# Kernel tuning notes

Hardware: AMD Instinct MI355X
Metric: run time of the kernel (lower is better)

The kernel has to match this reference:

```python
import jax, jax.numpy as jnp
import numpy as np

EMBED_DIM = 1024
NUM_HEADS = 16
HEAD_DIM = EMBED_DIM // NUM_HEADS


def setup_inputs() -> dict:
    key = jax.random.key(0)
    ks = jax.random.split(key, 7)
    B, S, E = 2, 2048, EMBED_DIM
    # xavier_uniform bound for square [E, E] weight
    bound = float(np.sqrt(6.0 / (E + E)))
    mkw = lambda k: jax.random.uniform(k, (E, E), jnp.float32, -bound, bound)
    return {
        "query": jax.random.normal(ks[0], (B, S, E), jnp.float32),
        "key": jax.random.normal(ks[1], (B, S, E), jnp.float32),
        "value": jax.random.normal(ks[2], (B, S, E), jnp.float32),
        "Wq": mkw(ks[3]),
        "Wk": mkw(ks[4]),
        "Wv": mkw(ks[5]),
        "Wo": mkw(ks[6]),
    }


def reference(query, key, value, Wq, Wk, Wv, Wo):
    # Chunked sigmoid attention: since sigmoid has no cross-key normalization
    # and all projections are bias-free linear maps, summing per-KV-chunk
    # partial outputs is mathematically identical to the full computation:
    #   out = (sigmoid(scale * Q K^T) @ V) @ Wo^T
    B, L, E = query.shape
    H, D = NUM_HEADS, HEAD_DIM
    scale = D ** -0.5
    q = (query @ Wq.T).reshape(B, L, H, D) * scale   # [B,L,H,D]
    k = (key @ Wk.T).reshape(B, -1, H, D)            # [B,S,H,D]
    v = (value @ Wv.T).reshape(B, -1, H, D)          # [B,S,H,D]
    scores = jax.nn.sigmoid(jnp.einsum('blhd,bshd->bhls', q, k))  # [B,H,L,S]
    o = jnp.einsum('bhls,bshd->blhd', scores, v).reshape(B, L, E)
    return o @ Wo.T
```

## Files before the change

kernel.cpp:

```cpp
#include <hip/hip_runtime.h>

typedef float f32x4 __attribute__((ext_vector_type(4)));
typedef float f32x16 __attribute__((ext_vector_type(16)));
typedef __bf16 bf16x4 __attribute__((ext_vector_type(4)));
typedef __bf16 bf16x8 __attribute__((ext_vector_type(8)));

constexpr int E = 1024;
constexpr int S = 2048;
constexpr int Bsz = 2;
constexpr int H = 16;
constexpr int Dh = 64;
constexpr int M = Bsz * S;
constexpr int E2 = 2048;

#define GLOAD_LDS16(g, l)                                                                 \
  __builtin_amdgcn_global_load_lds((const __attribute__((address_space(1))) void*)(g),    \
                                   (__attribute__((address_space(3))) void*)(l), 16, 0, 0)

__device__ __forceinline__ unsigned pk2(float a, float b) {
  union { __bf16 h[2]; unsigned u; } r;
  r.h[0] = (__bf16)a; r.h[1] = (__bf16)b;
  return r.u;
}

__global__ __launch_bounds__(256) void convert_bf16(
    const float* __restrict__ q, const float* __restrict__ k,
    const float* __restrict__ v, const float* __restrict__ wq,
    const float* __restrict__ wk, const float* __restrict__ wv,
    const float* __restrict__ wo, __bf16* __restrict__ aq,
    __bf16* __restrict__ ak, __bf16* __restrict__ av,
    __bf16* __restrict__ wqkv, __bf16* __restrict__ wob) {
  const int id = blockIdx.y;
  const float* src;
  __bf16* dst;
  int n;
  float scale = 1.0f;
  switch (id) {
    case 0: src = q;  dst = aq;             n = M * E; break;
    case 1: src = k;  dst = ak;             n = M * E; break;
    case 2: src = v;  dst = av;             n = M * E; break;
    case 3: src = wq; dst = wqkv;           n = E * E; scale = -0.18033688f; break;
    case 4: src = wk; dst = wqkv + E * E;   n = E * E; break;
    case 5: src = wv; dst = wqkv + 2 * E * E; n = E * E; break;
    default: src = wo; dst = wob;           n = E * E; break;
  }
  const int stride = gridDim.x * 256 * 8;
  for (int i = (blockIdx.x * 256 + threadIdx.x) * 8; i < n; i += stride) {
    f32x4 a = *reinterpret_cast<const f32x4*>(&src[i]);
    f32x4 b = *reinterpret_cast<const f32x4*>(&src[i + 4]);
    bf16x8 o;
    o[0] = (__bf16)(a[0] * scale); o[1] = (__bf16)(a[1] * scale);
    o[2] = (__bf16)(a[2] * scale); o[3] = (__bf16)(a[3] * scale);
    o[4] = (__bf16)(b[0] * scale); o[5] = (__bf16)(b[1] * scale);
    o[6] = (__bf16)(b[2] * scale); o[7] = (__bf16)(b[3] * scale);
    *reinterpret_cast<bf16x8*>(&dst[i]) = o;
  }
}

template <int TM, int MODE, int KS>
__global__ __launch_bounds__(256) void gemm_bf16nt(
    const __bf16* __restrict__ A0, const __bf16* __restrict__ A1,
    const __bf16* __restrict__ A2, const __bf16* __restrict__ Bw,
    void* __restrict__ C0, void* __restrict__ C1, void* __restrict__ C2) {
  constexpr int MI = TM / 32;
  __shared__ __bf16 As[TM][64];
  __shared__ __bf16 Bs[128][64];

  const int t    = threadIdx.x;
  const int lane = t & 63;
  const int wid  = t >> 6;
  const int wr   = (wid >> 1) * (TM / 2);
  const int wc   = (wid & 1) * 64;
  const int r16  = lane & 15;
  const int tm   = blockIdx.y * TM;
  const int tn   = blockIdx.x * 128;
  const int which = tn >> 10;

  const __bf16* Ab = (MODE == 0) ? (which == 0 ? A0 : which == 1 ? A1 : A2) : A0;

  f32x4 acc[MI][4] = {};

  for (int kt = 0; kt < KS / 64; ++kt) {
    const int k0  = kt * 64;
    const int k0b = k0 & 1023;
    __syncthreads();
    constexpr int ACH = TM / 8;
    constexpr int NCH = ACH + 16;
#pragma unroll
    for (int c = wid; c < NCH; c += 4) {
      const bool isA = c < ACH;
      const int cc   = isA ? c : c - ACH;
      const int L    = cc * 1024 + lane * 16;
      const int row  = L >> 7;
      const int sw   = ((L >> 4) & 7) ^ (row & 7);
      const __bf16* src = isA ? &Ab[(size_t)(tm + row) * KS + k0 + sw * 8]
                              : &Bw[(size_t)(tn + row) * 1024 + k0b + sw * 8];
      char* dst = (isA ? (char*)As : (char*)Bs) + cc * 1024;
      GLOAD_LDS16(src, dst);
    }
    __syncthreads();
#pragma unroll
    for (int kc = 0; kc < 2; ++kc) {
      bf16x8 af[MI], bfv[4];
#pragma unroll
      for (int mi = 0; mi < MI; ++mi) {
        int row = wr + mi * 16 + r16;
        int g   = (kc * 4 + (lane >> 4)) ^ (row & 7);
        af[mi] = *reinterpret_cast<const bf16x8*>(&As[row][g * 8]);
      }
#pragma unroll
      for (int ni = 0; ni < 4; ++ni) {
        int row = wc + ni * 16 + r16;
        int g   = (kc * 4 + (lane >> 4)) ^ (row & 7);
        bfv[ni] = *reinterpret_cast<const bf16x8*>(&Bs[row][g * 8]);
      }
#pragma unroll
      for (int mi = 0; mi < MI; ++mi)
#pragma unroll
        for (int ni = 0; ni < 4; ++ni)
          acc[mi][ni] = __builtin_amdgcn_mfma_f32_16x16x32_bf16(af[mi], bfv[ni],
                                                                acc[mi][ni], 0, 0, 0);
    }
  }

#pragma unroll
  for (int mi = 0; mi < MI; ++mi) {
#pragma unroll
    for (int ni = 0; ni < 4; ++ni) {
#pragma unroll
      for (int j = 0; j < 4; ++j) {
        float v = acc[mi][ni][j];
        int m = tm + wr + mi * 16 + ((lane >> 4) << 2) + j;
        int n = tn + wc + ni * 16 + r16;
        if constexpr (MODE == 0) {
          int nl = n & 1023;
          int b = m >> 11, s = m & 2047, h = nl >> 6, d = nl & 63;
          __bf16* Cout = which == 0 ? (__bf16*)C0 : which == 1 ? (__bf16*)C1
                                                              : (__bf16*)C2;
          if (which < 2) {
            Cout[((size_t)(b * H + h) * S + s) * Dh + d] = (__bf16)v;
          } else {
            int ssw = (s & ~12) | ((s & 4) << 1) | ((s & 8) >> 1);
            Cout[((size_t)(b * H + h) * Dh + d) * S + ssw] = (__bf16)v;
          }
        } else {
          ((float*)C0)[(size_t)m * E + n] = v;
        }
      }
    }
  }
}

__global__ __launch_bounds__(128, 4) void attn_sigmoid(const __bf16* __restrict__ Q,
                                                       const __bf16* __restrict__ K,
                                                       const __bf16* __restrict__ Vt,
                                                       __bf16* __restrict__ O) {
  __shared__ char smem[16384];

  const int t    = threadIdx.x;
  const int lane = t & 63;
  const int qgrp = t >> 6;
  const int l31  = lane & 31;
  const int hh   = lane >> 5;
  const int qt   = blockIdx.x >> 1;
  const int ss   = blockIdx.x & 1;
  const int q0   = qt * 64;
  const int h    = blockIdx.y;
  const int b    = blockIdx.z;

  const __bf16* Qh = Q + (size_t)(b * H + h) * S * Dh;
  const __bf16* Kh = K + (size_t)(b * H + h) * S * Dh;
  const __bf16* Vh = Vt + (size_t)(b * H + h) * Dh * S;

  const __bf16* kSrc = Kh + (size_t)(ss * 1024 + (lane >> 3)) * Dh +
                       (((lane & 7) ^ (lane >> 3)) * 8);
  const __bf16* vSrc = Vh + (size_t)(lane >> 2) * S + ss * 1024 +
                       (((lane & 3) ^ ((lane >> 3) & 3)) * 8);

  auto stage = [&](int it, int buf) {
    char* dst = smem + buf * 8192;
    if (qgrp == 0) {
#pragma unroll
      for (int j = 0; j < 4; ++j)
        GLOAD_LDS16(kSrc + it * 2048 + j * 512, dst + j * 1024);
    } else {
#pragma unroll
      for (int j = 0; j < 4; ++j)
        GLOAD_LDS16(vSrc + it * 32 + (size_t)j * 16 * S, dst + 4096 + j * 1024);
    }
  };

  bf16x8 Qf[4];
#pragma unroll
  for (int kc = 0; kc < 4; ++kc)
    Qf[kc] = *reinterpret_cast<const bf16x8*>(
        &Qh[(size_t)(q0 + qgrp * 32 + l31) * Dh + kc * 16 + hh * 8]);

  stage(0, 0);
  stage(1, 1);

  f32x16 ot0 = {}, ot1 = {};

#pragma unroll 2
  for (int it = 0; it < 32; ++it) {
    const int buf = it & 1;
    if (it + 1 < 32) {
      asm volatile("s_waitcnt vmcnt(4)" ::: "memory");
    } else {
      asm volatile("s_waitcnt vmcnt(0)" ::: "memory");
    }
    __builtin_amdgcn_s_barrier();
    __builtin_amdgcn_sched_barrier(0);

    const __bf16* Kb = (const __bf16*)(smem + buf * 8192);
    const __bf16* Vb = (const __bf16*)(smem + buf * 8192 + 4096);

    bf16x8 kf[4], vf[4];
#pragma unroll
    for (int kc = 0; kc < 4; ++kc) {
      int x = (2 * kc + hh) ^ (l31 & 7);
      kf[kc] = *reinterpret_cast<const bf16x8*>(&Kb[l31 * 64 + x * 8]);
    }
#pragma unroll
    for (int kc2 = 0; kc2 < 2; ++kc2)
#pragma unroll
      for (int dblk = 0; dblk < 2; ++dblk) {
        int row = dblk * 32 + l31;
        int x   = (2 * kc2 + hh) ^ ((l31 >> 1) & 3);
        vf[kc2 * 2 + dblk] = *reinterpret_cast<const bf16x8*>(&Vb[row * 32 + x * 8]);
      }

    f32x16 sacc = {};
    __builtin_amdgcn_s_setprio(1);
#pragma unroll
    for (int kc = 0; kc < 4; ++kc)
      sacc = __builtin_amdgcn_mfma_f32_32x32x16_bf16(kf[kc], Qf[kc], sacc, 0, 0, 0);
    __builtin_amdgcn_s_setprio(0);

    bf16x8 F[2];
    {
      union { unsigned u[4]; bf16x8 v; } fu[2];
#pragma unroll
      for (int kc2 = 0; kc2 < 2; ++kc2) {
#pragma unroll
        for (int jj = 0; jj < 4; ++jj) {
          float ya = sacc[kc2 * 8 + 2 * jj];
          float yb = sacc[kc2 * 8 + 2 * jj + 1];
          float pa = __builtin_amdgcn_rcpf(1.0f + __builtin_amdgcn_exp2f(ya));
          float pb = __builtin_amdgcn_rcpf(1.0f + __builtin_amdgcn_exp2f(yb));
          fu[kc2].u[jj] = pk2(pa, pb);
        }
        F[kc2] = fu[kc2].v;
      }
    }

    __builtin_amdgcn_s_setprio(1);
    ot0 = __builtin_amdgcn_mfma_f32_32x32x16_bf16(vf[0], F[0], ot0, 0, 0, 0);
    ot1 = __builtin_amdgcn_mfma_f32_32x32x16_bf16(vf[1], F[0], ot1, 0, 0, 0);
    ot0 = __builtin_amdgcn_mfma_f32_32x32x16_bf16(vf[2], F[1], ot0, 0, 0, 0);
    ot1 = __builtin_amdgcn_mfma_f32_32x32x16_bf16(vf[3], F[1], ot1, 0, 0, 0);
    __builtin_amdgcn_s_setprio(0);

    __builtin_amdgcn_sched_barrier(0);
    __builtin_amdgcn_s_barrier();
    if (it + 2 < 32) stage(it + 2, buf);
  }

  __bf16* Os = (__bf16*)smem;
  {
    int row = qgrp * 32 + l31;
#pragma unroll
    for (int dblk = 0; dblk < 2; ++dblk)
#pragma unroll
      for (int rp = 0; rp < 4; ++rp) {
        int r  = rp * 4;
        int g  = dblk * 4 + rp;
        int by = row * 128 + ((g ^ (row & 7)) * 16) + hh * 8;
        float a0 = dblk ? ot1[r]     : ot0[r];
        float a1 = dblk ? ot1[r + 1] : ot0[r + 1];
        float a2 = dblk ? ot1[r + 2] : ot0[r + 2];
        float a3 = dblk ? ot1[r + 3] : ot0[r + 3];
        unsigned long long val =
            (unsigned long long)pk2(a0, a1) | ((unsigned long long)pk2(a2, a3) << 32);
        *reinterpret_cast<unsigned long long*>((char*)Os + by) = val;
      }
  }
  __syncthreads();
#pragma unroll
  for (int i = 0; i < 4; ++i) {
    int c   = i * 128 + t;
    int row = c >> 3;
    int ch  = c & 7;
    bf16x8 v = *reinterpret_cast<const bf16x8*>(
        (char*)Os + row * 128 + ((ch ^ (row & 7)) * 16));
    *reinterpret_cast<bf16x8*>(
        &O[((size_t)(b * S) + q0 + row) * E2 + ss * 1024 + h * Dh + ch * 8]) = v;
  }
}

extern "C" void kernel_launch(void* const* d_in, const int* in_sizes, int n_in,
                              void* d_out, int out_size, void* d_ws, size_t ws_size,
                              hipStream_t stream) {
  const float* query = (const float*)d_in[0];
  const float* key_  = (const float*)d_in[1];
  const float* value = (const float*)d_in[2];
  const float* Wq    = (const float*)d_in[3];
  const float* Wk    = (const float*)d_in[4];
  const float* Wv    = (const float*)d_in[5];
  const float* Wo    = (const float*)d_in[6];

  char* ws = (char*)d_ws;
  __bf16* aq   = (__bf16*)(ws);
  __bf16* ak   = (__bf16*)(ws + ((size_t)8 << 20));
  __bf16* av   = (__bf16*)(ws + ((size_t)16 << 20));
  __bf16* wqkv = (__bf16*)(ws + ((size_t)24 << 20));
  __bf16* wob  = (__bf16*)(ws + ((size_t)30 << 20));
  __bf16* pq   = (__bf16*)(ws + ((size_t)32 << 20));
  __bf16* pk   = (__bf16*)(ws + ((size_t)40 << 20));
  __bf16* pvt  = (__bf16*)(ws + ((size_t)48 << 20));
  __bf16* ob   = (__bf16*)(ws);

  convert_bf16<<<dim3(512, 7), 256, 0, stream>>>(query, key_, value, Wq, Wk, Wv,
                                                 Wo, aq, ak, av, wqkv, wob);

  gemm_bf16nt<128, 0, 1024><<<dim3(3072 / 128, M / 128), 256, 0, stream>>>(
      aq, ak, av, wqkv, pq, pk, pvt);

  attn_sigmoid<<<dim3(S / 32, H, Bsz), 128, 0, stream>>>(pq, pk, pvt, ob);

  gemm_bf16nt<64, 2, 2048><<<dim3(E / 128, M / 64), 256, 0, stream>>>(
      ob, nullptr, nullptr, wob, (float*)d_out, nullptr, nullptr);
}
```

Measured before the change: 157.5 us.

## Double-buffer GEMM LDS loads with XCD-aware tile remap and smaller QKV tile

The GEMM kernel now double-buffers its LDS tiles, issuing async global-to-LDS loads two k-steps ahead and waiting with an explicit vmcnt. This lets memory traffic overlap the MFMA work instead of serializing on barriers. It also remaps the 1D block id so consecutive tiles land on the same XCD for L2 reuse, and raises MFMA wave priority with s_setprio. The QKV projection drops from 128-row to 64-row tiles to fit the new scheme, which doubles the number of workgroups and reduces per-block reuse. The hardcoded vmcnt literal is tied to TM=64.

```diff
diff --git a/kernel.cpp b/kernel.cpp
--- a/kernel.cpp
+++ b/kernel.cpp
@@ -62,9 +62,16 @@
     const __bf16* __restrict__ A0, const __bf16* __restrict__ A1,
     const __bf16* __restrict__ A2, const __bf16* __restrict__ Bw,
     void* __restrict__ C0, void* __restrict__ C1, void* __restrict__ C2) {
-  constexpr int MI = TM / 32;
-  __shared__ __bf16 As[TM][64];
-  __shared__ __bf16 Bs[128][64];
+  static_assert(TM == 64, "vmcnt literal assumes TM=64 (6 chunks/wave)");
+  constexpr int MI  = TM / 32;
+  constexpr int NT  = KS / 64;
+  constexpr int ACH = TM / 8;
+  constexpr int NCH = ACH + 16;
+  constexpr int NTN = (MODE == 0) ? 24 : 8;
+  constexpr int NWG = NTN * (M / TM);
+  constexpr int CPX = NWG / 8;
+
+  __shared__ char smem[2][NCH * 1024];
 
   const int t    = threadIdx.x;
   const int lane = t & 63;
@@ -72,20 +79,21 @@
   const int wr   = (wid >> 1) * (TM / 2);
   const int wc   = (wid & 1) * 64;
   const int r16  = lane & 15;
-  const int tm   = blockIdx.y * TM;
-  const int tn   = blockIdx.x * 128;
+
+  const int bid = blockIdx.x;
+  const int fid = (bid & 7) * CPX + (bid >> 3);
+  const int mt  = fid / NTN;
+  const int nt  = fid % NTN;
+  const int tm  = mt * TM;
+  const int tn  = nt * 128;
   const int which = tn >> 10;
 
   const __bf16* Ab = (MODE == 0) ? (which == 0 ? A0 : which == 1 ? A1 : A2) : A0;
 
-  f32x4 acc[MI][4] = {};
-
-  for (int kt = 0; kt < KS / 64; ++kt) {
+  auto stage = [&](int kt, int buf) {
     const int k0  = kt * 64;
     const int k0b = k0 & 1023;
-    __syncthreads();
-    constexpr int ACH = TM / 8;
-    constexpr int NCH = ACH + 16;
+    char* dst = smem[buf];
 #pragma unroll
     for (int c = wid; c < NCH; c += 4) {
       const bool isA = c < ACH;
@@ -95,10 +103,28 @@
       const int sw   = ((L >> 4) & 7) ^ (row & 7);
       const __bf16* src = isA ? &Ab[(size_t)(tm + row) * KS + k0 + sw * 8]
                               : &Bw[(size_t)(tn + row) * 1024 + k0b + sw * 8];
-      char* dst = (isA ? (char*)As : (char*)Bs) + cc * 1024;
-      GLOAD_LDS16(src, dst);
-    }
-    __syncthreads();
+      GLOAD_LDS16(src, dst + c * 1024);
+    }
+  };
+
+  stage(0, 0);
+  stage(1, 1);
+
+  f32x4 acc[MI][4] = {};
+
+  for (int kt = 0; kt < NT; ++kt) {
+    const int buf = kt & 1;
+    if (kt + 1 < NT) {
+      asm volatile("s_waitcnt vmcnt(6)" ::: "memory");
+    } else {
+      asm volatile("s_waitcnt vmcnt(0)" ::: "memory");
+    }
+    __builtin_amdgcn_s_barrier();
+    __builtin_amdgcn_sched_barrier(0);
+
+    const __bf16* As = (const __bf16*)smem[buf];
+    const __bf16* Bs = (const __bf16*)(smem[buf] + ACH * 1024);
+
 #pragma unroll
     for (int kc = 0; kc < 2; ++kc) {
       bf16x8 af[MI], bfv[4];
@@ -106,21 +132,27 @@
       for (int mi = 0; mi < MI; ++mi) {
         int row = wr + mi * 16 + r16;
         int g   = (kc * 4 + (lane >> 4)) ^ (row & 7);
-        af[mi] = *reinterpret_cast<const bf16x8*>(&As[row][g * 8]);
+        af[mi] = *reinterpret_cast<const bf16x8*>(&As[row * 64 + g * 8]);
       }
 #pragma unroll
       for (int ni = 0; ni < 4; ++ni) {
         int row = wc + ni * 16 + r16;
         int g   = (kc * 4 + (lane >> 4)) ^ (row & 7);
-        bfv[ni] = *reinterpret_cast<const bf16x8*>(&Bs[row][g * 8]);
-      }
+        bfv[ni] = *reinterpret_cast<const bf16x8*>(&Bs[row * 64 + g * 8]);
+      }
+      __builtin_amdgcn_s_setprio(1);
 #pragma unroll
       for (int mi = 0; mi < MI; ++mi)
 #pragma unroll
         for (int ni = 0; ni < 4; ++ni)
           acc[mi][ni] = __builtin_amdgcn_mfma_f32_16x16x32_bf16(af[mi], bfv[ni],
                                                                 acc[mi][ni], 0, 0, 0);
-    }
+      __builtin_amdgcn_s_setprio(0);
+    }
+
+    __builtin_amdgcn_sched_barrier(0);
+    __builtin_amdgcn_s_barrier();
+    if (kt + 2 < NT) stage(kt + 2, buf);
   }
 
 #pragma unroll
@@ -323,11 +355,11 @@
   convert_bf16<<<dim3(512, 7), 256, 0, stream>>>(query, key_, value, Wq, Wk, Wv,
                                                  Wo, aq, ak, av, wqkv, wob);
 
-  gemm_bf16nt<128, 0, 1024><<<dim3(3072 / 128, M / 128), 256, 0, stream>>>(
+  gemm_bf16nt<64, 0, 1024><<<1536, 256, 0, stream>>>(
       aq, ak, av, wqkv, pq, pk, pvt);
 
   attn_sigmoid<<<dim3(S / 32, H, Bsz), 128, 0, stream>>>(pq, pk, pvt, ob);
 
-  gemm_bf16nt<64, 2, 2048><<<dim3(E / 128, M / 64), 256, 0, stream>>>(
+  gemm_bf16nt<64, 2, 2048><<<512, 256, 0, stream>>>(
       ob, nullptr, nullptr, wob, (float*)d_out, nullptr, nullptr);
 }
```

New measurement: 144.8 us. 1.09x faster.
